# Kernel optimization log

Hardware: AMD Instinct MI355X
Metric: run time of the kernel (lower is better)

The kernel has to match this reference:

```python
import jax, jax.numpy as jnp
import numpy as np
from jax.scipy.special import logsumexp

B, T, D = 256, 2048, 64


def setup_inputs() -> dict:
    key = jax.random.key(0)
    k1, k2, k3, k4 = jax.random.split(key, 4)
    p = jax.random.normal(k1, (B, T, D), dtype=jnp.float32)
    labels = jax.random.randint(k2, (B, T), 0, D)
    y = jax.nn.one_hot(labels, D, dtype=jnp.int32)  # [B,T,D] one-hot labels
    # valid lengths in [T//2, T]; mask == 1 marks padding positions
    lengths = jax.random.randint(k3, (B,), T // 2, T + 1)
    mask = (jnp.arange(T)[None, :] >= lengths[:, None]).astype(jnp.int32)
    transition = 0.1 * jax.random.normal(k4, (D, D), dtype=jnp.float32)
    return {"p": p, "y": y, "mask": mask, "transition": transition}


def reference(p, y, mask, transition):
    # CRF negative log-likelihood per example: logZ - emission_score - transition_score
    Bb = p.shape[0]
    valid = (1 - mask).astype(jnp.float32)            # [B,T], 1 = valid token
    y1 = y.astype(jnp.float32) * valid[:, :, None]    # masked one-hot labels
    s1 = jnp.sum(y1 * p, axis=(1, 2))                 # emission score
    pair = jnp.einsum('btd,bte->bde', y1[:, :-1], y1[:, 1:])  # label bigram counts
    s2 = jnp.sum(pair * transition, axis=(1, 2))      # transition score

    # forward algorithm: alpha_t = p_t + logsumexp(alpha_{t-1}[:, :, None] + T)
    def step(state, inp):
        new = inp + logsumexp(state[:, :, None] + transition[None, :, :], axis=1)
        return new, new

    xs = jnp.moveaxis(p[:, 1:, :], 1, 0)              # [T-1, B, D]
    _, a1 = jax.lax.scan(step, p[:, 0, :], xs)        # a1: [T-1, B, D]

    # index of alpha at the last valid timestep (length L -> a1 index L-2)
    m1 = jnp.argmin(
        jnp.concatenate([valid.astype(jnp.int32), jnp.zeros((Bb, 1), jnp.int32)], axis=1),
        axis=1) - 2                                   # [B]
    last = a1[m1, jnp.arange(Bb)]                     # [B, D]
    logZ = logsumexp(last, axis=-1)
    return logZ - s1 - s2
```

## Files before the change

### kernel.cpp

```cpp
#include <hip/hip_runtime.h>
#include <stdint.h>
#include <string.h>

#define BB 256
#define TT 2048
#define DD 64
#define CC 64
#define SS 32
#define C_L2E 1.44269504f
#define C_LN2 0.69314718f
#define C_BIAS 0.0028174f

typedef short sh8  __attribute__((ext_vector_type(8)));
typedef float f32x4 __attribute__((ext_vector_type(4)));

union BU { sh8 v8; unsigned int u[4]; unsigned short s[8]; };

__device__ __forceinline__ float expf_fast(float x) { return __builtin_amdgcn_exp2f(x * C_L2E); }
__device__ __forceinline__ unsigned short bf16rne(float x) {
    unsigned int u = __float_as_uint(x);
    u += 0x7FFF + ((u >> 16) & 1u);
    return (unsigned short)(u >> 16);
}
__device__ __forceinline__ unsigned int pkbf(float hi, float lo) {
    return __builtin_amdgcn_perm(__float_as_uint(hi), __float_as_uint(lo), 0x07060302u);
}

#define DPPMAX(x, ctrl, rm, bm) { int _xi = __float_as_int(x);                              \
    int _yi = __builtin_amdgcn_update_dpp(_xi, _xi, ctrl, rm, bm, false);                   \
    x = fmaxf(x, __int_as_float(_yi)); }

__global__ __launch_bounds__(256) void crf_len(
    const int* __restrict__ mask, int* __restrict__ wsL)
{
    __shared__ int r4[4];
    const int c = blockIdx.x, tid = threadIdx.x;
    const int4* mrow = (const int4*)(mask + (size_t)c * TT);
    int4 a = mrow[tid * 2], b = mrow[tid * 2 + 1];
    int s = a.x + a.y + a.z + a.w + b.x + b.y + b.z + b.w;
#pragma unroll
    for (int xm = 32; xm >= 1; xm >>= 1) s += __shfl_xor(s, xm, 64);
    if ((tid & 63) == 0) r4[tid >> 6] = s;
    __syncthreads();
    if (tid == 0) wsL[c] = TT - (r4[0] + r4[1] + r4[2] + r4[3]);
}

__global__ __launch_bounds__(256) void crf_lab(
    const int* __restrict__ y, unsigned char* __restrict__ labsG)
{
    const int tid = threadIdx.x;
    const int g = tid & 15, sub = tid >> 4;
    const size_t base = (size_t)blockIdx.x * 64;
    int4 v[4];
#pragma unroll
    for (int k = 0; k < 4; ++k)
        v[k] = ((const int4*)y)[(base + (size_t)k * 16 + sub) * 16 + g];
#pragma unroll
    for (int k = 0; k < 4; ++k) {
        int s = v[k].x * (4 * g) + v[k].y * (4 * g + 1)
              + v[k].z * (4 * g + 2) + v[k].w * (4 * g + 3);
#pragma unroll
        for (int xm = 1; xm <= 8; xm <<= 1) s += __shfl_xor(s, xm, 16);
        if (g == 0) labsG[base + k * 16 + sub] = (unsigned char)s;
    }
}

__global__ __launch_bounds__(256) void crf_gth(
    const float* __restrict__ p, const unsigned char* __restrict__ labsG,
    const int* __restrict__ mask, const float* __restrict__ tr,
    float* __restrict__ wsS)
{
    __shared__ float redf[4];
    const int c = blockIdx.y, t0 = blockIdx.x * 256;
    const int tid = threadIdx.x;
    const size_t cb = (size_t)c * TT;
    const int tt = t0 + tid;

    const int m0 = mask[cb + tt];
    const int m1 = (tt + 1 < TT) ? mask[cb + tt + 1] : 1;
    const int l0 = labsG[cb + tt];

    float s = 0.f;
    if (m0 == 0)
        s += p[(cb + tt) * DD + l0];
    if (m1 == 0) {
        const int l1 = labsG[cb + tt + 1];
        s += tr[l0 * DD + l1];
    }
#pragma unroll
    for (int xm = 32; xm >= 1; xm >>= 1) s += __shfl_xor(s, xm, 64);
    if ((tid & 63) == 0) redf[tid >> 6] = s;
    __syncthreads();
    if (tid == 0)
        atomicAdd(&wsS[c], redf[0] + redf[1] + redf[2] + redf[3]);
}

__global__ __launch_bounds__(256) void crf_probe(
    const float* __restrict__ p, const float* __restrict__ tr,
    const int* __restrict__ wsL,
    unsigned short* __restrict__ wsA, unsigned short* __restrict__ wsB, int* __restrict__ wsSig)
{
    __shared__ char lds[4][2][4096];
    const int tid = threadIdx.x, w = tid >> 6, lane = tid & 63;
    const int q = lane >> 4, ml = lane & 15;
    const int cg = blockIdx.x;
    const int ic = blockIdx.y * 2 + (w >> 1);
    const int bwd = w & 1;
    const int c = cg * 16 + ml;
    const int Lml = wsL[c];
    const int t0 = ic * SS, t1 = t0 + SS;
    const int ts = (ic == 0) ? 1 : t0;
    const float* prow = p + (size_t)c * TT * DD;

    const int m4 = lane >> 4, u = lane & 15;
    const float* pb[4];
    int wr[4], rd[4];
#pragma unroll
    for (int k = 0; k < 4; ++k) {
        const int m = 4 * k + m4;
        const int su = (u ^ (m & 7)) << 4;
        pb[k] = p + (size_t)(cg * 16 + m) * TT * DD + (su >> 2);
        wr[k] = m * 256 + su;
        rd[k] = ml * 256 + (((4 * k + q) ^ (ml & 7)) << 4);
    }
    char* lbase = &lds[w][0][0];

    BU A[4][2];
#pragma unroll
    for (int mt = 0; mt < 4; ++mt)
#pragma unroll
        for (int kt2 = 0; kt2 < 2; ++kt2)
#pragma unroll
            for (int j = 0; j < 8; ++j) {
                int lam = 32 * kt2 + 16 * (j >> 2) + 4 * q + (j & 3);
                float tv = bwd ? tr[(16 * mt + ml) * DD + lam] : tr[lam * DD + 16 * mt + ml];
                A[mt][kt2].s[j] = (short)bf16rne(expf_fast(tv));
            }

    float xs[16];
    if (!bwd && ic == 0) {
#pragma unroll
        for (int k = 0; k < 4; ++k) {
            f32x4 v = *(const f32x4*)(prow + 16 * k + 4 * q);
#pragma unroll
            for (int r = 0; r < 4; ++r)
                xs[(k >> 1) * 8 + (k & 1) * 4 + r] = __builtin_amdgcn_exp2f(fmaf(v[r], C_L2E, C_BIAS));
        }
    } else {
#pragma unroll
        for (int i = 0; i < 16; ++i) xs[i] = 1.0f;
    }

    int mL = Lml;
#pragma unroll
    for (int xm = 32; xm >= 1; xm >>= 1) { int o = __shfl_xor(mL, xm, 64); mL = o > mL ? o : mL; }
    int ibeg = 0, iend = SS;
    if (!bwd) { int ir = mL - t0; if (ir < 0) ir = 0; iend = (ir + 3) & ~3; if (iend > SS) iend = SS; }
    else      { int ir = t1 - mL; if (ir < 0) ir = 0; ibeg = ir & ~3; if (ibeg > SS) ibeg = SS; }

    int sig = 0;
    const f32x4 z4 = {0.f, 0.f, 0.f, 0.f};

    if (ibeg < iend) {
        f32x4 gA[4], gB[4];
        {
            const int tp0 = bwd ? (t1 - 1 - ibeg) : (t0 + ibeg);
            f32x4 g0[4];
#pragma unroll
            for (int k = 0; k < 4; ++k)
                g0[k] = *(const f32x4*)(pb[k] + (size_t)tp0 * DD);
            int i1 = ibeg + 1;
            int tp1 = bwd ? (t1 - 1 - i1) : (t0 + i1);
            if (tp1 < t0) tp1 = t0;
            if (tp1 > t1 - 1) tp1 = t1 - 1;
#pragma unroll
            for (int k = 0; k < 4; ++k)
                gB[k] = *(const f32x4*)(pb[k] + (size_t)tp1 * DD);
#pragma unroll
            for (int k = 0; k < 4; ++k)
                *(f32x4*)(lbase + wr[k]) = g0[k];
        }

#define PSTEP(SE, RLOAD, RWRITE)                                                            \
        {                                                                                   \
            const int i = ib + SE;                                                          \
            const int t = bwd ? (t1 - 1 - i) : (t0 + i);                                    \
            const bool act = (t >= ts) && (t < Lml);                                        \
            {                                               \
                int ipf = i + 2;                                                            \
                int tpf = bwd ? (t1 - 1 - ipf) : (t0 + ipf);                                \
                if (tpf < t0) tpf = t0;                                                     \
                if (tpf > t1 - 1) tpf = t1 - 1;                                             \
                _Pragma("unroll")                                                           \
                for (int k = 0; k < 4; ++k)                                                 \
                    RLOAD[k] = *(const f32x4*)(pb[k] + (size_t)tpf * DD);                    \
            }                                                                               \
            f32x4 er[4];                                                                    \
            {                                  \
                char* lb = lbase + ((SE & 1) * 4096);                                       \
                _Pragma("unroll")                                                           \
                for (int k = 0; k < 4; ++k)                                                 \
                    er[k] = *(const f32x4*)(lb + rd[k]);                                    \
            }                                                                               \
            float ee[4][4];                                                                 \
            _Pragma("unroll")                                                               \
            for (int k = 0; k < 4; ++k)                                                     \
                _Pragma("unroll")                                                           \
                for (int r = 0; r < 4; ++r)                                                 \
                    ee[k][r] = __builtin_amdgcn_exp2f(fmaf(er[k][r], C_L2E, C_BIAS));       \
            float cand[16];                                                                 \
            BU Bf[2];                                                                       \
            f32x4 acc[4];                                                                   \
            if (!bwd) {                           \
                _Pragma("unroll")                                                           \
                for (int kt2 = 0; kt2 < 2; ++kt2)                                           \
                    _Pragma("unroll")                                                       \
                    for (int jj = 0; jj < 4; ++jj)                                          \
                        Bf[kt2].u[jj] = pkbf(xs[kt2 * 8 + 2 * jj + 1], xs[kt2 * 8 + 2 * jj]); \
                _Pragma("unroll")                                                           \
                for (int mt = 0; mt < 4; ++mt) {                                            \
                    acc[mt] = __builtin_amdgcn_mfma_f32_16x16x32_bf16(A[mt][0].v8, Bf[0].v8, z4, 0, 0, 0); \
                    acc[mt] = __builtin_amdgcn_mfma_f32_16x16x32_bf16(A[mt][1].v8, Bf[1].v8, acc[mt], 0, 0, 0); \
                }                                                                           \
                _Pragma("unroll")                                                           \
                for (int mt = 0; mt < 4; ++mt)                                              \
                    _Pragma("unroll")                                                       \
                    for (int r = 0; r < 4; ++r)                                             \
                        cand[(mt >> 1) * 8 + (mt & 1) * 4 + r] = acc[mt][r] * ee[mt][r];    \
            } else {                                  \
                float xsc[16];                                                              \
                _Pragma("unroll")                                                           \
                for (int kt2 = 0; kt2 < 2; ++kt2)                                           \
                    _Pragma("unroll")                                                       \
                    for (int h = 0; h < 2; ++h)                                             \
                        _Pragma("unroll")                                                   \
                        for (int r = 0; r < 4; ++r)                                         \
                            xsc[kt2 * 8 + h * 4 + r] = xs[kt2 * 8 + h * 4 + r] * ee[2 * kt2 + h][r]; \
                _Pragma("unroll")                                                           \
                for (int kt2 = 0; kt2 < 2; ++kt2)                                           \
                    _Pragma("unroll")                                                       \
                    for (int jj = 0; jj < 4; ++jj)                                          \
                        Bf[kt2].u[jj] = pkbf(xsc[kt2 * 8 + 2 * jj + 1], xsc[kt2 * 8 + 2 * jj]); \
                _Pragma("unroll")                                                           \
                for (int mt = 0; mt < 4; ++mt) {                                            \
                    acc[mt] = __builtin_amdgcn_mfma_f32_16x16x32_bf16(A[mt][0].v8, Bf[0].v8, z4, 0, 0, 0); \
                    acc[mt] = __builtin_amdgcn_mfma_f32_16x16x32_bf16(A[mt][1].v8, Bf[1].v8, acc[mt], 0, 0, 0); \
                }                                                                           \
                _Pragma("unroll")                                                           \
                for (int mt = 0; mt < 4; ++mt)                                              \
                    _Pragma("unroll")                                                       \
                    for (int r = 0; r < 4; ++r)                                             \
                        cand[(mt >> 1) * 8 + (mt & 1) * 4 + r] = acc[mt][r];                \
            }                                                                               \
            {                    \
                char* lw = lbase + ((1 - (SE & 1)) * 4096);                                 \
                _Pragma("unroll")                                                           \
                for (int k = 0; k < 4; ++k)                                                 \
                    *(f32x4*)(lw + wr[k]) = RWRITE[k];                                      \
            }                                                                               \
            if (SE == 3) {                    \
                float mx = fabsf(cand[0]);                                                  \
                _Pragma("unroll")                                                           \
                for (int i2 = 1; i2 < 16; ++i2) mx = fmaxf(mx, fabsf(cand[i2]));            \
                DPPMAX(mx, 0x111, 0xF, 0xF); DPPMAX(mx, 0x112, 0xF, 0xF);                   \
                DPPMAX(mx, 0x114, 0xF, 0xF); DPPMAX(mx, 0x118, 0xF, 0xF);                   \
                DPPMAX(mx, 0x142, 0xA, 0xF); DPPMAX(mx, 0x143, 0xC, 0xF);                   \
                int smx = __builtin_amdgcn_readlane(__float_as_int(mx), 63);                \
                int kk = ((smx >> 23) & 255) - 127;                                         \
                kk = kk < -124 ? -124 : (kk > 124 ? 124 : kk);                              \
                float sc = __int_as_float((unsigned)(127 - kk) << 23);                      \
                _Pragma("unroll")                                                           \
                for (int i2 = 0; i2 < 16; ++i2) cand[i2] *= sc;                             \
                if (act) sig += kk;                                                         \
            }                                                                               \
            _Pragma("unroll")                                                               \
            for (int i2 = 0; i2 < 16; ++i2) xs[i2] = act ? cand[i2] : xs[i2];               \
        }

        for (int ib = ibeg; ib < iend; ib += 4) {
            PSTEP(0, gA, gB)
            PSTEP(1, gB, gA)
            PSTEP(2, gA, gB)
            PSTEP(3, gB, gA)
        }
#undef PSTEP
    }

    unsigned short* dst = (bwd ? wsB : wsA) + ((size_t)c * CC + ic) * 64;
#pragma unroll
    for (int kt2 = 0; kt2 < 2; ++kt2)
#pragma unroll
        for (int h = 0; h < 2; ++h)
#pragma unroll
            for (int r = 0; r < 4; ++r)
                dst[32 * kt2 + 16 * h + 4 * q + r] = bf16rne(xs[kt2 * 8 + h * 4 + r]);
    if (!bwd && q == 0) wsSig[c * CC + ic] = sig;
}

__global__ __launch_bounds__(256) void crf_combine(
    const unsigned short* __restrict__ wsA, const unsigned short* __restrict__ wsB,
    const int* __restrict__ wsSig, const float* __restrict__ wsS,
    float* __restrict__ out)
{
    __shared__ float eParts[4];
    const int tid = threadIdx.x, w = tid >> 6, lane = tid & 63;
    const int c = blockIdx.x;

    float Ep = 0.f;
#pragma unroll
    for (int k = 0; k < 16; ++k) {
        const int i = w * 16 + k;
        if (i == 0) continue;
        float b  = __uint_as_float((unsigned)wsB[((size_t)c * CC + i) * 64 + lane] << 16);
        float ap = __uint_as_float((unsigned)wsA[((size_t)c * CC + i - 1) * 64 + lane] << 16);
        float d1 = b * ap, d0 = b;
#pragma unroll
        for (int xm = 32; xm >= 1; xm >>= 1) { d1 += __shfl_xor(d1, xm, 64); d0 += __shfl_xor(d0, xm, 64); }
        Ep += (float)wsSig[c * CC + i] + __builtin_amdgcn_logf(d1) - __builtin_amdgcn_logf(d0);
    }
    if (w == 0) Ep += (float)wsSig[c * CC];
    if (w == 3) {
        float al = __uint_as_float((unsigned)wsA[((size_t)c * CC + CC - 1) * 64 + lane] << 16);
#pragma unroll
        for (int xm = 32; xm >= 1; xm >>= 1) al += __shfl_xor(al, xm, 64);
        Ep += __builtin_amdgcn_logf(al);
    }
    if (lane == 0) eParts[w] = Ep;
    __syncthreads();
    if (tid == 0) {
        float E = eParts[0] + eParts[1] + eParts[2] + eParts[3];
        out[c] = C_LN2 * E - wsS[c];
    }
}

extern "C" void kernel_launch(void* const* d_in, const int* in_sizes, int n_in,
                              void* d_out, int out_size, void* d_ws, size_t ws_size,
                              hipStream_t stream) {
    const float* p  = (const float*)d_in[0];
    const int*   y  = (const int*)d_in[1];
    const int*   mk = (const int*)d_in[2];
    const float* tr = (const float*)d_in[3];
    float* out = (float*)d_out;

    float* wsS  = (float*)d_ws;
    int*   wsL  = (int*)((char*)d_ws + 1024);
    int*   wsSg = (int*)((char*)d_ws + 4096);
    unsigned char* wsLb = (unsigned char*)((char*)d_ws + 131072);
    unsigned short* wsA = (unsigned short*)((char*)d_ws + (1u << 20));
    unsigned short* wsB = (unsigned short*)((char*)d_ws + (3u << 20));

    hipMemsetAsync(d_ws, 0, 1024, stream);
    crf_len<<<dim3(BB), dim3(256), 0, stream>>>(mk, wsL);
    crf_lab<<<dim3(BB * TT / 64), dim3(256), 0, stream>>>(y, wsLb);
    crf_probe<<<dim3(16, CC / 2), dim3(256), 0, stream>>>(p, tr, wsL, wsA, wsB, wsSg);
    crf_gth<<<dim3(8, BB), dim3(256), 0, stream>>>(p, wsLb, mk, tr, wsS);
    crf_combine<<<dim3(BB), dim3(256), 0, stream>>>(wsA, wsB, wsSg, wsS, out);
}
```

Before: 317.7 us.

## Interleave two independent time chunks per wave and drop LDS staging

The time axis is split into 128 chunks of 16 steps instead of 64 of 32, and each wave now runs two independent chunk recurrences (A and B) interleaved step by step. This hides MFMA and exp latency along the serial dependency chain. The emission rows are now loaded straight from global memory into registers instead of being staged through swizzled LDS, which removes LDS writes and reads. The costs are higher register pressure, less coalesced global loads, twice as many chunk boundaries for the combine kernel to process, and chunk B's range uses A's length-based early-exit bounds.

```diff
diff --git a/kernel.cpp b/kernel.cpp
--- a/kernel.cpp
+++ b/kernel.cpp
@@ -5,8 +5,8 @@
 #define BB 256
 #define TT 2048
 #define DD 64
-#define CC 64
-#define SS 32
+#define CC 128
+#define SS 16
 #define C_L2E 1.44269504f
 #define C_LN2 0.69314718f
 #define C_BIAS 0.0028174f
@@ -100,30 +100,19 @@
     const int* __restrict__ wsL,
     unsigned short* __restrict__ wsA, unsigned short* __restrict__ wsB, int* __restrict__ wsSig)
 {
-    __shared__ char lds[4][2][4096];
     const int tid = threadIdx.x, w = tid >> 6, lane = tid & 63;
     const int q = lane >> 4, ml = lane & 15;
     const int cg = blockIdx.x;
-    const int ic = blockIdx.y * 2 + (w >> 1);
+    const int icA = blockIdx.y * 4 + (w >> 1) * 2;
+    const int icB = icA + 1;
     const int bwd = w & 1;
     const int c = cg * 16 + ml;
     const int Lml = wsL[c];
-    const int t0 = ic * SS, t1 = t0 + SS;
-    const int ts = (ic == 0) ? 1 : t0;
+    const int t0A = icA * SS, t1A = t0A + SS;
+    const int t0B = icB * SS, t1B = t0B + SS;
+    const int tsA = (icA == 0) ? 1 : t0A;
+    const int tsB = t0B;
     const float* prow = p + (size_t)c * TT * DD;
-
-    const int m4 = lane >> 4, u = lane & 15;
-    const float* pb[4];
-    int wr[4], rd[4];
-#pragma unroll
-    for (int k = 0; k < 4; ++k) {
-        const int m = 4 * k + m4;
-        const int su = (u ^ (m & 7)) << 4;
-        pb[k] = p + (size_t)(cg * 16 + m) * TT * DD + (su >> 2);
-        wr[k] = m * 256 + su;
-        rd[k] = ml * 256 + (((4 * k + q) ^ (ml & 7)) << 4);
-    }
-    char* lbase = &lds[w][0][0];
 
     BU A[4][2];
 #pragma unroll
@@ -137,77 +126,66 @@
                 A[mt][kt2].s[j] = (short)bf16rne(expf_fast(tv));
             }
 
-    float xs[16];
-    if (!bwd && ic == 0) {
+    float xsA[16], xsB[16];
+    if (!bwd && icA == 0) {
 #pragma unroll
         for (int k = 0; k < 4; ++k) {
             f32x4 v = *(const f32x4*)(prow + 16 * k + 4 * q);
 #pragma unroll
             for (int r = 0; r < 4; ++r)
-                xs[(k >> 1) * 8 + (k & 1) * 4 + r] = __builtin_amdgcn_exp2f(fmaf(v[r], C_L2E, C_BIAS));
+                xsA[(k >> 1) * 8 + (k & 1) * 4 + r] = __builtin_amdgcn_exp2f(fmaf(v[r], C_L2E, C_BIAS));
         }
     } else {
 #pragma unroll
-        for (int i = 0; i < 16; ++i) xs[i] = 1.0f;
-    }
+        for (int i = 0; i < 16; ++i) xsA[i] = 1.0f;
+    }
+#pragma unroll
+    for (int i = 0; i < 16; ++i) xsB[i] = 1.0f;
 
     int mL = Lml;
 #pragma unroll
     for (int xm = 32; xm >= 1; xm >>= 1) { int o = __shfl_xor(mL, xm, 64); mL = o > mL ? o : mL; }
-    int ibeg = 0, iend = SS;
-    if (!bwd) { int ir = mL - t0; if (ir < 0) ir = 0; iend = (ir + 3) & ~3; if (iend > SS) iend = SS; }
-    else      { int ir = t1 - mL; if (ir < 0) ir = 0; ibeg = ir & ~3; if (ibeg > SS) ibeg = SS; }
-
-    int sig = 0;
+    int ibegU = 0, iendU = SS;
+    if (!bwd) { int ir = mL - t0A; if (ir < 0) ir = 0; iendU = (ir + 3) & ~3; if (iendU > SS) iendU = SS; }
+    else      { int ir = t1A - mL; if (ir < 0) ir = 0; ibegU = ir & ~3; if (ibegU > SS) ibegU = SS; }
+
+    int sigA = 0, sigB = 0;
     const f32x4 z4 = {0.f, 0.f, 0.f, 0.f};
 
-    if (ibeg < iend) {
-        f32x4 gA[4], gB[4];
-        {
-            const int tp0 = bwd ? (t1 - 1 - ibeg) : (t0 + ibeg);
-            f32x4 g0[4];
-#pragma unroll
-            for (int k = 0; k < 4; ++k)
-                g0[k] = *(const f32x4*)(pb[k] + (size_t)tp0 * DD);
-            int i1 = ibeg + 1;
-            int tp1 = bwd ? (t1 - 1 - i1) : (t0 + i1);
-            if (tp1 < t0) tp1 = t0;
-            if (tp1 > t1 - 1) tp1 = t1 - 1;
-#pragma unroll
-            for (int k = 0; k < 4; ++k)
-                gB[k] = *(const f32x4*)(pb[k] + (size_t)tp1 * DD);
-#pragma unroll
-            for (int k = 0; k < 4; ++k)
-                *(f32x4*)(lbase + wr[k]) = g0[k];
+    if (ibegU < iendU) {
+        f32x4 erA[2][4], erB[2][4];
+#pragma unroll
+        for (int s = 0; s < 2; ++s) {
+            int i = ibegU + s;
+            int tA = bwd ? (t1A - 1 - i) : (t0A + i);
+            int tB = bwd ? (t1B - 1 - i) : (t0B + i);
+#pragma unroll
+            for (int k = 0; k < 4; ++k) {
+                erA[s][k] = *(const f32x4*)(prow + (size_t)tA * DD + 16 * k + 4 * q);
+                erB[s][k] = *(const f32x4*)(prow + (size_t)tB * DD + 16 * k + 4 * q);
+            }
         }
 
-#define PSTEP(SE, RLOAD, RWRITE)                                                            \
+#define PSTEP(X, SE)                                                                        \
         {                                                                                   \
             const int i = ib + SE;                                                          \
-            const int t = bwd ? (t1 - 1 - i) : (t0 + i);                                    \
-            const bool act = (t >= ts) && (t < Lml);                                        \
-            {                                               \
-                int ipf = i + 2;                                                            \
-                int tpf = bwd ? (t1 - 1 - ipf) : (t0 + ipf);                                \
-                if (tpf < t0) tpf = t0;                                                     \
-                if (tpf > t1 - 1) tpf = t1 - 1;                                             \
-                _Pragma("unroll")                                                           \
-                for (int k = 0; k < 4; ++k)                                                 \
-                    RLOAD[k] = *(const f32x4*)(pb[k] + (size_t)tpf * DD);                    \
-            }                                                                               \
-            f32x4 er[4];                                                                    \
-            {                                  \
-                char* lb = lbase + ((SE & 1) * 4096);                                       \
-                _Pragma("unroll")                                                           \
-                for (int k = 0; k < 4; ++k)                                                 \
-                    er[k] = *(const f32x4*)(lb + rd[k]);                                    \
-            }                                                                               \
+            const int t = bwd ? (t1##X - 1 - i) : (t0##X + i);                              \
+            const bool act = (t >= ts##X) && (t < Lml);                                     \
             float ee[4][4];                                                                 \
             _Pragma("unroll")                                                               \
             for (int k = 0; k < 4; ++k)                                                     \
                 _Pragma("unroll")                                                           \
                 for (int r = 0; r < 4; ++r)                                                 \
-                    ee[k][r] = __builtin_amdgcn_exp2f(fmaf(er[k][r], C_L2E, C_BIAS));       \
+                    ee[k][r] = __builtin_amdgcn_exp2f(fmaf(er##X[SE & 1][k][r], C_L2E, C_BIAS)); \
+            {                                             \
+                int ipf = i + 2;                                                            \
+                int tpf = bwd ? (t1##X - 1 - ipf) : (t0##X + ipf);                          \
+                if (tpf < t0##X) tpf = t0##X;                                               \
+                if (tpf > t1##X - 1) tpf = t1##X - 1;                                       \
+                _Pragma("unroll")                                                           \
+                for (int k = 0; k < 4; ++k)                                                 \
+                    er##X[SE & 1][k] = *(const f32x4*)(prow + (size_t)tpf * DD + 16 * k + 4 * q); \
+            }                                                                               \
             float cand[16];                                                                 \
             BU Bf[2];                                                                       \
             f32x4 acc[4];                                                                   \
@@ -216,7 +194,7 @@
                 for (int kt2 = 0; kt2 < 2; ++kt2)                                           \
                     _Pragma("unroll")                                                       \
                     for (int jj = 0; jj < 4; ++jj)                                          \
-                        Bf[kt2].u[jj] = pkbf(xs[kt2 * 8 + 2 * jj + 1], xs[kt2 * 8 + 2 * jj]); \
+                        Bf[kt2].u[jj] = pkbf(xs##X[kt2 * 8 + 2 * jj + 1], xs##X[kt2 * 8 + 2 * jj]); \
                 _Pragma("unroll")                                                           \
                 for (int mt = 0; mt < 4; ++mt) {                                            \
                     acc[mt] = __builtin_amdgcn_mfma_f32_16x16x32_bf16(A[mt][0].v8, Bf[0].v8, z4, 0, 0, 0); \
@@ -235,7 +213,7 @@
                     for (int h = 0; h < 2; ++h)                                             \
                         _Pragma("unroll")                                                   \
                         for (int r = 0; r < 4; ++r)                                         \
-                            xsc[kt2 * 8 + h * 4 + r] = xs[kt2 * 8 + h * 4 + r] * ee[2 * kt2 + h][r]; \
+                            xsc[kt2 * 8 + h * 4 + r] = xs##X[kt2 * 8 + h * 4 + r] * ee[2 * kt2 + h][r]; \
                 _Pragma("unroll")                                                           \
                 for (int kt2 = 0; kt2 < 2; ++kt2)                                           \
                     _Pragma("unroll")                                                       \
@@ -251,12 +229,6 @@
                     _Pragma("unroll")                                                       \
                     for (int r = 0; r < 4; ++r)                                             \
                         cand[(mt >> 1) * 8 + (mt & 1) * 4 + r] = acc[mt][r];                \
-            }                                                                               \
-            {                    \
-                char* lw = lbase + ((1 - (SE & 1)) * 4096);                                 \
-                _Pragma("unroll")                                                           \
-                for (int k = 0; k < 4; ++k)                                                 \
-                    *(f32x4*)(lw + wr[k]) = RWRITE[k];                                      \
             }                                                                               \
             if (SE == 3) {                    \
                 float mx = fabsf(cand[0]);                                                  \
@@ -271,30 +243,36 @@
                 float sc = __int_as_float((unsigned)(127 - kk) << 23);                      \
                 _Pragma("unroll")                                                           \
                 for (int i2 = 0; i2 < 16; ++i2) cand[i2] *= sc;                             \
-                if (act) sig += kk;                                                         \
+                if (act) sig##X += kk;                                                      \
             }                                                                               \
             _Pragma("unroll")                                                               \
-            for (int i2 = 0; i2 < 16; ++i2) xs[i2] = act ? cand[i2] : xs[i2];               \
+            for (int i2 = 0; i2 < 16; ++i2) xs##X[i2] = act ? cand[i2] : xs##X[i2];         \
         }
 
-        for (int ib = ibeg; ib < iend; ib += 4) {
-            PSTEP(0, gA, gB)
-            PSTEP(1, gB, gA)
-            PSTEP(2, gA, gB)
-            PSTEP(3, gB, gA)
+        for (int ib = ibegU; ib < iendU; ib += 4) {
+            PSTEP(A, 0) PSTEP(B, 0)
+            PSTEP(A, 1) PSTEP(B, 1)
+            PSTEP(A, 2) PSTEP(B, 2)
+            PSTEP(A, 3) PSTEP(B, 3)
         }
 #undef PSTEP
     }
 
-    unsigned short* dst = (bwd ? wsB : wsA) + ((size_t)c * CC + ic) * 64;
+    unsigned short* dstA = (bwd ? wsB : wsA) + ((size_t)c * CC + icA) * 64;
+    unsigned short* dstB = (bwd ? wsB : wsA) + ((size_t)c * CC + icB) * 64;
 #pragma unroll
     for (int kt2 = 0; kt2 < 2; ++kt2)
 #pragma unroll
         for (int h = 0; h < 2; ++h)
 #pragma unroll
-            for (int r = 0; r < 4; ++r)
-                dst[32 * kt2 + 16 * h + 4 * q + r] = bf16rne(xs[kt2 * 8 + h * 4 + r]);
-    if (!bwd && q == 0) wsSig[c * CC + ic] = sig;
+            for (int r = 0; r < 4; ++r) {
+                dstA[32 * kt2 + 16 * h + 4 * q + r] = bf16rne(xsA[kt2 * 8 + h * 4 + r]);
+                dstB[32 * kt2 + 16 * h + 4 * q + r] = bf16rne(xsB[kt2 * 8 + h * 4 + r]);
+            }
+    if (!bwd && q == 0) {
+        wsSig[c * CC + icA] = sigA;
+        wsSig[c * CC + icB] = sigB;
+    }
 }
 
 __global__ __launch_bounds__(256) void crf_combine(
@@ -307,9 +285,9 @@
     const int c = blockIdx.x;
 
     float Ep = 0.f;
-#pragma unroll
-    for (int k = 0; k < 16; ++k) {
-        const int i = w * 16 + k;
+#pragma unroll 4
+    for (int k = 0; k < CC / 4; ++k) {
+        const int i = w * (CC / 4) + k;
         if (i == 0) continue;
         float b  = __uint_as_float((unsigned)wsB[((size_t)c * CC + i) * 64 + lane] << 16);
         float ap = __uint_as_float((unsigned)wsA[((size_t)c * CC + i - 1) * 64 + lane] << 16);
@@ -345,14 +323,14 @@
     float* wsS  = (float*)d_ws;
     int*   wsL  = (int*)((char*)d_ws + 1024);
     int*   wsSg = (int*)((char*)d_ws + 4096);
-    unsigned char* wsLb = (unsigned char*)((char*)d_ws + 131072);
+    unsigned char* wsLb = (unsigned char*)((char*)d_ws + 262144);
     unsigned short* wsA = (unsigned short*)((char*)d_ws + (1u << 20));
-    unsigned short* wsB = (unsigned short*)((char*)d_ws + (3u << 20));
+    unsigned short* wsB = (unsigned short*)((char*)d_ws + (5u << 20));
 
     hipMemsetAsync(d_ws, 0, 1024, stream);
     crf_len<<<dim3(BB), dim3(256), 0, stream>>>(mk, wsL);
     crf_lab<<<dim3(BB * TT / 64), dim3(256), 0, stream>>>(y, wsLb);
-    crf_probe<<<dim3(16, CC / 2), dim3(256), 0, stream>>>(p, tr, wsL, wsA, wsB, wsSg);
+    crf_probe<<<dim3(16, CC / 4), dim3(256), 0, stream>>>(p, tr, wsL, wsA, wsB, wsSg);
     crf_gth<<<dim3(8, BB), dim3(256), 0, stream>>>(p, wsLb, mk, tr, wsS);
     crf_combine<<<dim3(BB), dim3(256), 0, stream>>>(wsA, wsB, wsSg, wsS, out);
 }
```

Measured after the change: 327.9 us. 3.2% more time.
